# Optimization experiments

Hardware: AMD Instinct MI355X
Metric: run time of the kernel (lower is better)

The kernel has to match this reference:

```python
import jax, jax.numpy as jnp
import numpy as np

K, P, D = 9, 4, 1          # kernel_size, padding, dilation of each WeightedConv1D (stride=1)
SIGMA = 0.08               # WeightedConv1D default; the sigma arg of WeightedConv2D.forward is ignored
EPS = 1e-5                 # BatchNorm1d eps


def setup_inputs() -> dict:
    key = jax.random.key(0)
    ks = jax.random.split(key, 9)
    B, C, O, N = 4, 64, 64, 16384
    return {
        "input": jax.random.normal(ks[0], (B, C, N), jnp.float32),
        "multi_coords": jax.random.uniform(ks[1], (B, 3, N, 4), dtype=jnp.float32),
        "indices": jax.random.randint(ks[2], (B, N, 4), 0, N),
        "reindices": jax.random.randint(ks[3], (B, N, 4), 0, N),
        "conv_w": jax.random.normal(ks[4], (4, O, C, K), jnp.float32) * 0.05,   # 4 WeightedConv1D weights [O,C,K]
        "fusion_w": jax.random.normal(ks[5], (O, 4 * O), jnp.float32) * 0.05,   # Conv1d(4O -> O, kernel=1)
        "fusion_b": jax.random.normal(ks[6], (O,), jnp.float32) * 0.05,
        "bn_gamma": jnp.ones((O,), jnp.float32),
        "bn_beta": jnp.zeros((O,), jnp.float32),
    }


def _weighted_conv1d(x, coords, w):
    """x: [B,C,N], coords: [B,3,N], w: [O,C,K] -> [B,O,N] (L == N since P = D*(K-1)/2)."""
    N = x.shape[-1]
    win = jnp.arange(N)[None, :] + jnp.arange(K)[:, None] * D          # [K, N] window gather indices
    xw = jnp.pad(x, ((0, 0), (0, 0), (P, P)))[:, :, win]               # [B,C,K,N] == F.unfold layout
    cw = jnp.pad(coords, ((0, 0), (0, 0), (P, P)))[:, :, win]          # [B,3,K,N]
    diff = cw - cw[:, :, K // 2 : K // 2 + 1, :]                        # subtract window-center coord
    dw = jnp.maximum(1.0 - jnp.sqrt(jnp.sum(diff * diff, axis=1)) / SIGMA, 0.0)  # [B,K,N]
    return jnp.einsum('bckn,ock->bon', xw * dw[:, None], w)


def reference(input, multi_coords, indices, reindices, conv_w, fusion_w, fusion_b, bn_gamma, bn_beta):
    x = input
    outs = []
    for i in range(4):  # 4 space-filling-curve orderings; note x is reassigned (gathers compound)
        x = jnp.take_along_axis(x, indices[:, None, :, i], axis=2)      # [B,C,N]
        y = _weighted_conv1d(x, multi_coords[:, :, :, i], conv_w[i])    # [B,O,N]
        y = jnp.take_along_axis(y, reindices[:, None, :, i], axis=2)
        outs.append(y)
    cat = jnp.concatenate(outs, axis=1)                                 # [B,4O,N]
    # fusion: Conv1d(4O,O,kernel=1,padding=1,stride=1) -> padded positions see only bias
    z = jnp.einsum('bcn,oc->bon', cat, fusion_w)
    z = jnp.pad(z, ((0, 0), (0, 0), (1, 1))) + fusion_b[None, :, None]  # [B,O,N+2]
    # BatchNorm1d (training-mode batch statistics, biased variance)
    mean = jnp.mean(z, axis=(0, 2), keepdims=True)
    var = jnp.var(z, axis=(0, 2), keepdims=True)
    z = (z - mean) / jnp.sqrt(var + EPS) * bn_gamma[None, :, None] + bn_beta[None, :, None]
    return jax.nn.relu(z)
```

## Files before the change

kernel.cpp:

```cpp
#include <hip/hip_runtime.h>

#define K_ 9
#define SIGMA_INV 12.5f
#define EPS 1e-5f
#define B_ 4
#define C_ 64
#define O_ 64
#define N_ 16384
#define CAP 32768

typedef __attribute__((ext_vector_type(8))) short short8;
typedef __attribute__((ext_vector_type(4))) float f32x4;

__device__ __forceinline__ unsigned short f2bf(float f) {
    union { float f; unsigned u; } v; v.f = f;
    unsigned r = v.u + 0x7fffu + ((v.u >> 16) & 1u);
    return (unsigned short)(r >> 16);
}
__device__ __forceinline__ float bf2f(unsigned short h) {
    union { unsigned u; float f; } v; v.u = ((unsigned)h) << 16;
    return v.f;
}
__device__ __forceinline__ void gload16(const void* g, void* l) {
    __builtin_amdgcn_global_load_lds((const __attribute__((address_space(1))) unsigned int*)g,
                                     (__attribute__((address_space(3))) unsigned int*)l,
                                     16, 0, 0);
}

__global__ __launch_bounds__(256) void k_chain(const int* __restrict__ indices,
                                               const int* __restrict__ reidx,
                                               int* __restrict__ h,
                                               int* __restrict__ cnt) {
    int gid = blockIdx.x * 256 + threadIdx.x;
    if (gid == 0) *cnt = 0;
    int b = gid >> 14, n = gid & (N_ - 1);
    const int* ib = indices + (size_t)b * N_ * 4;
    const int4 r = *(const int4*)&reidx[((size_t)b * N_ + n) * 4];
    int t0 = ib[(size_t)r.x * 4 + 0];
    int t1 = ib[(size_t)r.y * 4 + 1];
    int t2 = ib[(size_t)r.z * 4 + 2];
    int t3 = ib[(size_t)r.w * 4 + 3];
    t1 = ib[(size_t)t1 * 4 + 0];
    t2 = ib[(size_t)t2 * 4 + 1];
    t3 = ib[(size_t)t3 * 4 + 2];
    t2 = ib[(size_t)t2 * 4 + 0];
    t3 = ib[(size_t)t3 * 4 + 1];
    t3 = ib[(size_t)t3 * 4 + 0];
    h[(size_t)(0 * 4 + b) * N_ + n] = t0;
    h[(size_t)(1 * 4 + b) * N_ + n] = t1;
    h[(size_t)(2 * 4 + b) * N_ + n] = t2;
    h[(size_t)(3 * 4 + b) * N_ + n] = t3;
}

__global__ __launch_bounds__(256) void k_setup(
    const float* __restrict__ in, const float* __restrict__ mc,
    const float* __restrict__ cw, const float* __restrict__ fw,
    unsigned short* __restrict__ xtb,
    unsigned short* __restrict__ Mfrag, float* __restrict__ Wt,
    float* __restrict__ FWt,
    int* __restrict__ flag, int* __restrict__ emeta,
    float* __restrict__ ed, int* __restrict__ cnt)
{
    int bid = blockIdx.x, t = threadIdx.x;
    if (bid < 1024) {
        __shared__ float tile[64][65];
        int b = bid & 3, n0 = (bid >> 2) * 64;
        for (int rep = 0; rep < 16; ++rep) {
            int idx = rep * 256 + t;
            int c = idx >> 6, j = idx & 63;
            tile[c][j] = in[((size_t)b * C_ + c) * N_ + n0 + j];
        }
        __syncthreads();
        for (int rep = 0; rep < 4; ++rep) {
            int idx = rep * 256 + t;
            int j = idx >> 4, c4 = (idx & 15) * 4;
            ushort4 o;
            o.x = f2bf(tile[c4 + 0][j]); o.y = f2bf(tile[c4 + 1][j]);
            o.z = f2bf(tile[c4 + 2][j]); o.w = f2bf(tile[c4 + 3][j]);
            *(ushort4*)&xtb[((size_t)b * N_ + n0 + j) * 64 + c4] = o;
        }
    } else if (bid < 1280) {
        __shared__ float cs[3][264][4];
        int sb = bid - 1024;
        int b = sb & 3, n0 = (sb >> 2) * 256;
        for (int idx = t; idx < 3 * 264; idx += 256) {
            int a = idx / 264, r = idx - a * 264;
            int m = n0 + r - 4;
            f32x4 v;
            if (m >= 0 && m < N_) v = *(const f32x4*)&mc[(((size_t)b * 3 + a) * N_ + m) * 4];
            else { v[0] = 1e9f; v[1] = 1e9f; v[2] = 1e9f; v[3] = 1e9f; }
            *(f32x4*)&cs[a][r][0] = v;
        }
        __syncthreads();
        int p = n0 + t;
        for (int i = 0; i < 4; ++i) {
            float c0 = cs[0][t + 4][i], c1 = cs[1][t + 4][i], c2 = cs[2][t + 4][i];
            float d[8]; bool any = false;
            #pragma unroll
            for (int kk = 0; kk < 8; ++kk) {
                int k = kk + (kk >= 4);
                float d0 = cs[0][t + k][i] - c0, d1 = cs[1][t + k][i] - c1,
                      d2 = cs[2][t + k][i] - c2;
                float dist = sqrtf(d0 * d0 + d1 * d1 + d2 * d2);
                float dd = 1.f - dist * SIGMA_INV;
                d[kk] = dd > 0.f ? dd : 0.f;
                any = any || (dd > 0.f);
            }
            int fv = 0;
            if (any) {
                int e = atomicAdd(cnt, 1);
                if (e < CAP) {
                    emeta[e] = ((i * 4 + b) << 14) | p;
                    #pragma unroll
                    for (int kk = 0; kk < 8; ++kk) ed[(size_t)e * 8 + kk] = d[kk];
                    fv = e + 1;
                }
            }
            flag[(size_t)(i * 4 + b) * N_ + p] = fv;
        }
    } else {
        int pb = bid - 1280;
        if (pb < 4) {
            __shared__ float w4[64][65];
            __shared__ float fws[64][65];
            int i = pb;
            for (int idx = t; idx < 4096; idx += 256) {
                int op = idx >> 6, c = idx & 63;
                w4[op][c]  = cw[(((size_t)(i * 64 + op)) * 64 + c) * 9 + 4];
                fws[op][c] = fw[(size_t)op * 256 + i * 64 + c];
            }
            __syncthreads();
            int o = t >> 2, cb = (t & 3) * 16;
            float acc[16];
            #pragma unroll
            for (int j = 0; j < 16; ++j) acc[j] = 0.f;
            for (int op = 0; op < 64; ++op) {
                float f = fws[o][op];
                #pragma unroll
                for (int j = 0; j < 16; ++j) acc[j] += f * w4[op][cb + j];
            }
            #pragma unroll
            for (int j = 0; j < 16; ++j) {
                int c = cb + j;
                int s = i * 2 + (c >> 5);
                int l = (((c >> 3) & 3) << 4) | (o & 15);
                int w_ = o >> 4;
                Mfrag[(((size_t)w_ * 8 + s) * 64 + l) * 8 + (c & 7)] = f2bf(acc[j]);
            }
        } else if (pb < 40) {
            int idx2 = pb - 4;
            int i = idx2 / 9, k = idx2 - i * 9;
            for (int idx = t; idx < 4096; idx += 256) {
                int c = idx >> 6, o = idx & 63;
                Wt[(size_t)(i * 9 + k) * 4096 + c * 64 + o] =
                    cw[(((size_t)(i * 64 + o)) * 64 + c) * 9 + k];
            }
        } else {
            int i = pb - 40;
            for (int idx = t; idx < 4096; idx += 256) {
                int c = idx >> 6, o = idx & 63;
                FWt[(size_t)(i * 64 + c) * 64 + o] = fw[(size_t)o * 256 + i * 64 + c];
            }
        }
    }
}

__global__ __launch_bounds__(64) void k_corr(
    const unsigned short* __restrict__ xtb, const int* __restrict__ indices,
    const float* __restrict__ Wt, const float* __restrict__ FWt,
    const int* __restrict__ emeta, const float* __restrict__ ed,
    const int* __restrict__ cnt, float* __restrict__ zcorr)
{
    __shared__ float xls[8][64];
    __shared__ float ycs[64];
    __shared__ int rows_s[8];
    int t = threadIdx.x;
    int n = *cnt; if (n > CAP) n = CAP;
    for (int e = blockIdx.x; e < n; e += gridDim.x) {
        int meta = emeta[e];
        int ibx = meta >> 14, p = meta & 16383;
        int i = ibx >> 2, b = ibx & 3;
        const int* idxb = indices + (size_t)b * N_ * 4;
        float dd[8];
        #pragma unroll
        for (int kk = 0; kk < 8; ++kk) dd[kk] = ed[(size_t)e * 8 + kk];
        if (t < 8) {
            int row = 0;
            if (dd[t] > 0.f) {
                int k = t + (t >= 4);
                int rr = p + k - 4;
                for (int s = i; s >= 0; --s) rr = idxb[(size_t)rr * 4 + s];
                row = rr;
            }
            rows_s[t] = row;
        }
        __syncthreads();
        #pragma unroll
        for (int kk = 0; kk < 8; ++kk) {
            if (dd[kk] > 0.f)
                xls[kk][t] = bf2f(xtb[((size_t)b * N_ + rows_s[kk]) * 64 + t]);
        }
        __syncthreads();
        float y = 0.f;
        #pragma unroll 1
        for (int kk = 0; kk < 8; ++kk) {
            if (dd[kk] > 0.f) {
                int k = kk + (kk >= 4);
                const float* w = Wt + (size_t)(i * 9 + k) * 4096;
                float s0 = 0.f, s1 = 0.f, s2 = 0.f, s3 = 0.f;
                #pragma unroll
                for (int c = 0; c < 64; c += 4) {
                    s0 += w[(c + 0) * 64 + t] * xls[kk][c + 0];
                    s1 += w[(c + 1) * 64 + t] * xls[kk][c + 1];
                    s2 += w[(c + 2) * 64 + t] * xls[kk][c + 2];
                    s3 += w[(c + 3) * 64 + t] * xls[kk][c + 3];
                }
                y += dd[kk] * (((s0 + s1) + (s2 + s3)));
            }
        }
        ycs[t] = y;
        __syncthreads();
        const float* fwt = FWt + (size_t)i * 4096;
        float v0 = 0.f, v1 = 0.f, v2 = 0.f, v3 = 0.f;
        #pragma unroll
        for (int c = 0; c < 64; c += 4) {
            v0 += fwt[(c + 0) * 64 + t] * ycs[c + 0];
            v1 += fwt[(c + 1) * 64 + t] * ycs[c + 1];
            v2 += fwt[(c + 2) * 64 + t] * ycs[c + 2];
            v3 += fwt[(c + 3) * 64 + t] * ycs[c + 3];
        }
        zcorr[(size_t)e * 64 + t] = (v0 + v1) + (v2 + v3);
        __syncthreads();
    }
}

__global__ __launch_bounds__(256) void k_fused(
    const unsigned short* __restrict__ xtb, const int* __restrict__ h,
    const int* __restrict__ flag, const int* __restrict__ reidx,
    const unsigned short* __restrict__ Mfrag, const float* __restrict__ zcorr,
    const float* __restrict__ fb, float* __restrict__ zbuf,
    float* __restrict__ pstats)
{
    __shared__ __align__(16) unsigned short xg[256 * 64];
    __shared__ int fs[256];
    int bid = blockIdx.x;
    int b = (bid & 7) >> 1;
    int nb = ((bid >> 3) << 1) | (bid & 1);
    int n0 = nb * 64;
    int t = threadIdx.x;
    int lane = t & 63, w = t >> 6;

    int hvv[8];
    #pragma unroll
    for (int it = 0; it < 8; ++it)
        hvv[it] = h[(size_t)(w * 4 + b) * N_ + n0 + it * 8 + (lane >> 3)];
    short8 af[8];
    #pragma unroll
    for (int s = 0; s < 8; ++s)
        af[s] = *(const short8*)&Mfrag[(((size_t)w * 8 + s) * 64 + lane) * 8];
    #pragma unroll
    for (int it = 0; it < 8; ++it) {
        int p = it * 8 + (lane >> 3);
        int cg = (lane & 7) ^ (p & 7);
        const unsigned short* gp = xtb + ((size_t)b * N_ + hvv[it]) * 64 + cg * 8;
        gload16(gp, &xg[(size_t)(w * 64 + it * 8) * 64]);
    }
    {
        int i = t >> 6, p = t & 63;
        int pr = reidx[((size_t)b * N_ + n0 + p) * 4 + i];
        fs[t] = flag[(size_t)(i * 4 + b) * N_ + pr];
    }
    asm volatile("s_waitcnt vmcnt(0)" ::: "memory");
    __syncthreads();

    f32x4 acc[4];
    #pragma unroll
    for (int ct = 0; ct < 4; ++ct) { acc[ct][0]=0.f; acc[ct][1]=0.f; acc[ct][2]=0.f; acc[ct][3]=0.f; }
    #pragma unroll
    for (int s = 0; s < 8; ++s) {
        int i2 = s >> 1;
        int cg = (s & 1) * 4 + (lane >> 4);
        #pragma unroll
        for (int ct = 0; ct < 4; ++ct) {
            int pos = ct * 16 + (lane & 15);
            const short8 bf = *(const short8*)((const char*)xg +
                ((size_t)(i2 * 64 + pos) * 128) + ((cg ^ (pos & 7)) * 16));
            acc[ct] = __builtin_amdgcn_mfma_f32_16x16x32_bf16(af[s], bf, acc[ct], 0, 0, 0);
        }
    }

    int og = w * 16 + (lane >> 4) * 4;
    const f32x4 bias4 = *(const f32x4*)&fb[og];
    float sums[4] = {0.f, 0.f, 0.f, 0.f}, sqs[4] = {0.f, 0.f, 0.f, 0.f};
    #pragma unroll
    for (int ct = 0; ct < 4; ++ct) {
        int p = ct * 16 + (lane & 15);
        #pragma unroll
        for (int i = 0; i < 4; ++i) {
            int f = fs[i * 64 + p];
            if (f > 0) {
                const f32x4 vc = *(const f32x4*)&zcorr[(size_t)(f - 1) * 64 + og];
                acc[ct] += vc;
            }
        }
        f32x4 z = acc[ct] + bias4;
        int n = n0 + p;
        #pragma unroll
        for (int r = 0; r < 4; ++r) {
            zbuf[((size_t)b * O_ + og + r) * N_ + n] = z[r];
            sums[r] += z[r]; sqs[r] += z[r] * z[r];
        }
    }
    #pragma unroll
    for (int r = 0; r < 4; ++r) {
        float s = sums[r], q = sqs[r];
        for (int m = 8; m >= 1; m >>= 1) {
            s += __shfl_xor(s, m);
            q += __shfl_xor(q, m);
        }
        if ((lane & 15) == 0) {
            pstats[(size_t)(og + r) * 1024 + bid] = s;
            pstats[(size_t)(64 + og + r) * 1024 + bid] = q;
        }
    }
}

__global__ __launch_bounds__(256) void k_bnstats(
    const float* __restrict__ pstats, const float* __restrict__ fb,
    const float* __restrict__ gamma, const float* __restrict__ beta,
    float* __restrict__ sc)
{
    __shared__ float ls[4], lq[4];
    int o = blockIdx.x, t = threadIdx.x;
    int lane = t & 63, w = t >> 6;
    float s = 0.f, q = 0.f;
    #pragma unroll
    for (int r = 0; r < 4; ++r) {
        s += pstats[(size_t)o * 1024 + r * 256 + t];
        q += pstats[(size_t)(64 + o) * 1024 + r * 256 + t];
    }
    #pragma unroll
    for (int m = 32; m >= 1; m >>= 1) {
        s += __shfl_xor(s, m);
        q += __shfl_xor(q, m);
    }
    if (lane == 0) { ls[w] = s; lq[w] = q; }
    __syncthreads();
    if (t == 0) {
        s = ls[0] + ls[1] + ls[2] + ls[3];
        q = lq[0] + lq[1] + lq[2] + lq[3];
        float cnt = (float)(B_ * (N_ + 2));
        float bias = fb[o];
        s += 2.f * B_ * bias;
        q += 2.f * B_ * bias * bias;
        float mean = s / cnt;
        float var = q / cnt - mean * mean;
        float scale = gamma[o] / sqrtf(var + EPS);
        sc[o] = scale;
        sc[O_ + o] = beta[o] - mean * scale;
    }
}

__global__ __launch_bounds__(256) void k_apply(const float* __restrict__ zbuf,
                                               const float* __restrict__ fb,
                                               const float* __restrict__ sc,
                                               float* __restrict__ out) {
    int bid = blockIdx.x, t = threadIdx.x;
    if (bid < 4096) {
        int gid = bid * 256 + t;
        int row = gid >> 12;
        int n = (gid & 4095) * 4;
        int o = row & 63;
        float scale = sc[o], shift = sc[O_ + o];
        f32x4 z = *(const f32x4*)&zbuf[(size_t)row * N_ + n];
        size_t ob = (size_t)row * (N_ + 2) + 1 + n;
        #pragma unroll
        for (int r = 0; r < 4; ++r)
            out[ob + r] = fmaxf(z[r] * scale + shift, 0.f);
    } else {
        int row = t;
        int o = row & 63;
        float v = fmaxf(fb[o] * sc[o] + sc[O_ + o], 0.f);
        out[(size_t)row * (N_ + 2)] = v;
        out[(size_t)row * (N_ + 2) + N_ + 1] = v;
    }
}

extern "C" void kernel_launch(void* const* d_in, const int* in_sizes, int n_in,
                              void* d_out, int out_size, void* d_ws, size_t ws_size,
                              hipStream_t stream) {
    const float* input   = (const float*)d_in[0];
    const float* mc      = (const float*)d_in[1];
    const int*   indices = (const int*)d_in[2];
    const int*   reidx   = (const int*)d_in[3];
    const float* cw      = (const float*)d_in[4];
    const float* fw      = (const float*)d_in[5];
    const float* fb      = (const float*)d_in[6];
    const float* gamma   = (const float*)d_in[7];
    const float* beta    = (const float*)d_in[8];
    float* out = (float*)d_out;

    char* ws = (char*)d_ws;
    size_t off = 0;
    auto alloc = [&](size_t bytes) { void* p = ws + off; off += (bytes + 255) & ~(size_t)255; return p; };
    unsigned short* xtb = (unsigned short*)alloc((size_t)B_ * N_ * C_ * 2);
    int*   h     = (int*)  alloc((size_t)4 * B_ * N_ * 4);
    unsigned short* Mfrag = (unsigned short*)alloc((size_t)4 * 8 * 64 * 8 * 2);
    float* Wt    = (float*)alloc((size_t)4 * 9 * 4096 * 4);
    float* FWt   = (float*)alloc((size_t)4 * 4096 * 4);
    int*   emeta = (int*)  alloc((size_t)CAP * 4);
    float* ed    = (float*)alloc((size_t)CAP * 8 * 4);
    float* zcorr = (float*)alloc((size_t)CAP * 64 * 4);
    float* zbuf  = (float*)alloc((size_t)B_ * O_ * N_ * 4);
    float* pstats= (float*)alloc((size_t)128 * 1024 * 4);
    float* sc    = (float*)alloc((size_t)128 * 4);
    int*   flag  = (int*)  alloc((size_t)4 * B_ * N_ * 4);
    int*   cnt   = (int*)  alloc(256);

    k_chain<<<256, 256, 0, stream>>>(indices, reidx, h, cnt);
    k_setup<<<1324, 256, 0, stream>>>(input, mc, cw, fw,
                                      xtb, Mfrag, Wt, FWt, flag, emeta, ed, cnt);
    k_corr<<<2048, 64, 0, stream>>>(xtb, indices, Wt, FWt, emeta, ed, cnt, zcorr);
    k_fused<<<1024, 256, 0, stream>>>(xtb, h, flag, reidx, Mfrag, zcorr, fb, zbuf, pstats);
    k_bnstats<<<64, 256, 0, stream>>>(pstats, fb, gamma, beta, sc);
    k_apply<<<4097, 256, 0, stream>>>(zbuf, fb, sc, out);
}
```

Measured before the change: 69.11 us.

## Fuse fusion GEMM, BN stats and apply into cooperative kernel with grid syncs

Merges the fused GEMM, batch-norm statistics and normalize/ReLU stages into one cooperative kernel that keeps accumulators in registers across two grid-wide syncs. This removes the full zbuf round trip through global memory and two kernel launches. It also folds the index-chain kernel into the setup kernel and swaps the single global atomic compaction counter for per-block local counters with fixed-capacity regions. The risks are that more than RCAP active points in one block are silently dropped, that grid-sync and occupancy requirements apply, and that a non-cooperative fallback path is kept.

```diff
diff --git a/kernel.cpp b/kernel.cpp
--- a/kernel.cpp
+++ b/kernel.cpp
@@ -1,4 +1,7 @@
 #include <hip/hip_runtime.h>
+#include <hip/hip_cooperative_groups.h>
+
+namespace cg = cooperative_groups;
 
 #define K_ 9
 #define SIGMA_INV 12.5f
@@ -7,7 +10,7 @@
 #define C_ 64
 #define O_ 64
 #define N_ 16384
-#define CAP 32768
+#define RCAP 128
 
 typedef __attribute__((ext_vector_type(8))) short short8;
 typedef __attribute__((ext_vector_type(4))) float f32x4;
@@ -27,39 +30,15 @@
                                      16, 0, 0);
 }
 
-__global__ __launch_bounds__(256) void k_chain(const int* __restrict__ indices,
-                                               const int* __restrict__ reidx,
-                                               int* __restrict__ h,
-                                               int* __restrict__ cnt) {
-    int gid = blockIdx.x * 256 + threadIdx.x;
-    if (gid == 0) *cnt = 0;
-    int b = gid >> 14, n = gid & (N_ - 1);
-    const int* ib = indices + (size_t)b * N_ * 4;
-    const int4 r = *(const int4*)&reidx[((size_t)b * N_ + n) * 4];
-    int t0 = ib[(size_t)r.x * 4 + 0];
-    int t1 = ib[(size_t)r.y * 4 + 1];
-    int t2 = ib[(size_t)r.z * 4 + 2];
-    int t3 = ib[(size_t)r.w * 4 + 3];
-    t1 = ib[(size_t)t1 * 4 + 0];
-    t2 = ib[(size_t)t2 * 4 + 1];
-    t3 = ib[(size_t)t3 * 4 + 2];
-    t2 = ib[(size_t)t2 * 4 + 0];
-    t3 = ib[(size_t)t3 * 4 + 1];
-    t3 = ib[(size_t)t3 * 4 + 0];
-    h[(size_t)(0 * 4 + b) * N_ + n] = t0;
-    h[(size_t)(1 * 4 + b) * N_ + n] = t1;
-    h[(size_t)(2 * 4 + b) * N_ + n] = t2;
-    h[(size_t)(3 * 4 + b) * N_ + n] = t3;
-}
-
 __global__ __launch_bounds__(256) void k_setup(
     const float* __restrict__ in, const float* __restrict__ mc,
+    const int* __restrict__ indices, const int* __restrict__ reidx,
     const float* __restrict__ cw, const float* __restrict__ fw,
-    unsigned short* __restrict__ xtb,
+    unsigned short* __restrict__ xtb, int* __restrict__ h,
     unsigned short* __restrict__ Mfrag, float* __restrict__ Wt,
     float* __restrict__ FWt,
     int* __restrict__ flag, int* __restrict__ emeta,
-    float* __restrict__ ed, int* __restrict__ cnt)
+    float* __restrict__ ed, int* __restrict__ bcnt)
 {
     int bid = blockIdx.x, t = threadIdx.x;
     if (bid < 1024) {
@@ -81,8 +60,10 @@
         }
     } else if (bid < 1280) {
         __shared__ float cs[3][264][4];
+        __shared__ int lcnt;
         int sb = bid - 1024;
         int b = sb & 3, n0 = (sb >> 2) * 256;
+        if (t == 0) lcnt = 0;
         for (int idx = t; idx < 3 * 264; idx += 256) {
             int a = idx / 264, r = idx - a * 264;
             int m = n0 + r - 4;
@@ -108,17 +89,20 @@
             }
             int fv = 0;
             if (any) {
-                int e = atomicAdd(cnt, 1);
-                if (e < CAP) {
-                    emeta[e] = ((i * 4 + b) << 14) | p;
+                int li = atomicAdd(&lcnt, 1);
+                if (li < RCAP) {
+                    int slot = sb * RCAP + li;
+                    emeta[slot] = (i << 14) | p;
                     #pragma unroll
-                    for (int kk = 0; kk < 8; ++kk) ed[(size_t)e * 8 + kk] = d[kk];
-                    fv = e + 1;
+                    for (int kk = 0; kk < 8; ++kk) ed[(size_t)slot * 8 + kk] = d[kk];
+                    fv = slot + 1;
                 }
             }
             flag[(size_t)(i * 4 + b) * N_ + p] = fv;
         }
-    } else {
+        __syncthreads();
+        if (t == 0) bcnt[sb] = lcnt < RCAP ? lcnt : RCAP;
+    } else if (bid < 1324) {
         int pb = bid - 1280;
         if (pb < 4) {
             __shared__ float w4[64][65];
@@ -162,6 +146,25 @@
                 FWt[(size_t)(i * 64 + c) * 64 + o] = fw[(size_t)o * 256 + i * 64 + c];
             }
         }
+    } else {
+        int gid = (bid - 1324) * 256 + t;
+        int b = gid >> 14, n = gid & (N_ - 1);
+        const int* ib = indices + (size_t)b * N_ * 4;
+        const int4 r = *(const int4*)&reidx[((size_t)b * N_ + n) * 4];
+        int t0 = ib[(size_t)r.x * 4 + 0];
+        int t1 = ib[(size_t)r.y * 4 + 1];
+        int t2 = ib[(size_t)r.z * 4 + 2];
+        int t3 = ib[(size_t)r.w * 4 + 3];
+        t1 = ib[(size_t)t1 * 4 + 0];
+        t2 = ib[(size_t)t2 * 4 + 1];
+        t3 = ib[(size_t)t3 * 4 + 2];
+        t2 = ib[(size_t)t2 * 4 + 0];
+        t3 = ib[(size_t)t3 * 4 + 1];
+        t3 = ib[(size_t)t3 * 4 + 0];
+        h[(size_t)(0 * 4 + b) * N_ + n] = t0;
+        h[(size_t)(1 * 4 + b) * N_ + n] = t1;
+        h[(size_t)(2 * 4 + b) * N_ + n] = t2;
+        h[(size_t)(3 * 4 + b) * N_ + n] = t3;
     }
 }
 
@@ -169,21 +172,23 @@
     const unsigned short* __restrict__ xtb, const int* __restrict__ indices,
     const float* __restrict__ Wt, const float* __restrict__ FWt,
     const int* __restrict__ emeta, const float* __restrict__ ed,
-    const int* __restrict__ cnt, float* __restrict__ zcorr)
+    const int* __restrict__ bcnt, float* __restrict__ zcorr)
 {
     __shared__ float xls[8][64];
     __shared__ float ycs[64];
     __shared__ int rows_s[8];
     int t = threadIdx.x;
-    int n = *cnt; if (n > CAP) n = CAP;
-    for (int e = blockIdx.x; e < n; e += gridDim.x) {
-        int meta = emeta[e];
-        int ibx = meta >> 14, p = meta & 16383;
-        int i = ibx >> 2, b = ibx & 3;
-        const int* idxb = indices + (size_t)b * N_ * 4;
+    int r = blockIdx.x >> 3, wir = blockIdx.x & 7;
+    int b = r & 3;
+    int cr = bcnt[r];
+    const int* idxb = indices + (size_t)b * N_ * 4;
+    for (int li = wir; li < cr; li += 8) {
+        int slot = r * RCAP + li;
+        int meta = emeta[slot];
+        int i = meta >> 14, p = meta & 16383;
         float dd[8];
         #pragma unroll
-        for (int kk = 0; kk < 8; ++kk) dd[kk] = ed[(size_t)e * 8 + kk];
+        for (int kk = 0; kk < 8; ++kk) dd[kk] = ed[(size_t)slot * 8 + kk];
         if (t < 8) {
             int row = 0;
             if (dd[t] > 0.f) {
@@ -229,12 +234,165 @@
             v2 += fwt[(c + 2) * 64 + t] * ycs[c + 2];
             v3 += fwt[(c + 3) * 64 + t] * ycs[c + 3];
         }
-        zcorr[(size_t)e * 64 + t] = (v0 + v1) + (v2 + v3);
-        __syncthreads();
-    }
-}
-
-__global__ __launch_bounds__(256) void k_fused(
+        zcorr[(size_t)slot * 64 + t] = (v0 + v1) + (v2 + v3);
+        __syncthreads();
+    }
+}
+
+__global__ __launch_bounds__(256, 2) void k_mega2(
+    const unsigned short* __restrict__ xtb, const int* __restrict__ h,
+    const int* __restrict__ flag, const int* __restrict__ reidx,
+    const unsigned short* __restrict__ Mfrag, const float* __restrict__ zcorr,
+    const float* __restrict__ fb, const float* __restrict__ gamma,
+    const float* __restrict__ beta, float* __restrict__ pstats,
+    float* __restrict__ sc, float* __restrict__ out)
+{
+    __shared__ __align__(16) unsigned short xg[2][256 * 64];
+    __shared__ int fs[2][256];
+    __shared__ float red_s[4], red_q[4];
+    int bid = blockIdx.x;
+    int b = bid & 3;
+    int base = (bid >> 2) * 128;
+    int t = threadIdx.x;
+    int lane = t & 63, w = t >> 6;
+
+    short8 af[8];
+    #pragma unroll
+    for (int s = 0; s < 8; ++s)
+        af[s] = *(const short8*)&Mfrag[(((size_t)w * 8 + s) * 64 + lane) * 8];
+    #pragma unroll
+    for (int j = 0; j < 2; ++j) {
+        int n0 = base + j * 64;
+        int hvv[8];
+        #pragma unroll
+        for (int it = 0; it < 8; ++it)
+            hvv[it] = h[(size_t)(w * 4 + b) * N_ + n0 + it * 8 + (lane >> 3)];
+        #pragma unroll
+        for (int it = 0; it < 8; ++it) {
+            int p = it * 8 + (lane >> 3);
+            int cg = (lane & 7) ^ (p & 7);
+            const unsigned short* gp = xtb + ((size_t)b * N_ + hvv[it]) * 64 + cg * 8;
+            gload16(gp, &xg[j][(size_t)(w * 64 + it * 8) * 64]);
+        }
+        {
+            int i = t >> 6, p = t & 63;
+            int pr = reidx[((size_t)b * N_ + n0 + p) * 4 + i];
+            fs[j][t] = flag[(size_t)(i * 4 + b) * N_ + pr];
+        }
+    }
+    asm volatile("s_waitcnt vmcnt(0)" ::: "memory");
+    __syncthreads();
+
+    f32x4 acc[2][4];
+    #pragma unroll
+    for (int j = 0; j < 2; ++j)
+        #pragma unroll
+        for (int ct = 0; ct < 4; ++ct) { acc[j][ct][0]=0.f; acc[j][ct][1]=0.f; acc[j][ct][2]=0.f; acc[j][ct][3]=0.f; }
+    #pragma unroll
+    for (int j = 0; j < 2; ++j)
+        #pragma unroll
+        for (int s = 0; s < 8; ++s) {
+            int i2 = s >> 1;
+            int cg = (s & 1) * 4 + (lane >> 4);
+            #pragma unroll
+            for (int ct = 0; ct < 4; ++ct) {
+                int pos = ct * 16 + (lane & 15);
+                const short8 bf = *(const short8*)((const char*)&xg[j][0] +
+                    ((size_t)(i2 * 64 + pos) * 128) + ((cg ^ (pos & 7)) * 16));
+                acc[j][ct] = __builtin_amdgcn_mfma_f32_16x16x32_bf16(af[s], bf, acc[j][ct], 0, 0, 0);
+            }
+        }
+
+    int og = w * 16 + (lane >> 4) * 4;
+    const f32x4 bias4 = *(const f32x4*)&fb[og];
+    float sums[4] = {0.f, 0.f, 0.f, 0.f}, sqs[4] = {0.f, 0.f, 0.f, 0.f};
+    #pragma unroll
+    for (int j = 0; j < 2; ++j)
+        #pragma unroll
+        for (int ct = 0; ct < 4; ++ct) {
+            int p = ct * 16 + (lane & 15);
+            #pragma unroll
+            for (int i = 0; i < 4; ++i) {
+                int f = fs[j][i * 64 + p];
+                if (f > 0) {
+                    const f32x4 vc = *(const f32x4*)&zcorr[(size_t)(f - 1) * 64 + og];
+                    acc[j][ct] += vc;
+                }
+            }
+            acc[j][ct] += bias4;
+            #pragma unroll
+            for (int r = 0; r < 4; ++r) { sums[r] += acc[j][ct][r]; sqs[r] += acc[j][ct][r] * acc[j][ct][r]; }
+        }
+    #pragma unroll
+    for (int r = 0; r < 4; ++r) {
+        float s = sums[r], q = sqs[r];
+        for (int m = 8; m >= 1; m >>= 1) {
+            s += __shfl_xor(s, m);
+            q += __shfl_xor(q, m);
+        }
+        if ((lane & 15) == 0) {
+            pstats[(size_t)(og + r) * 512 + bid] = s;
+            pstats[(size_t)(64 + og + r) * 512 + bid] = q;
+        }
+    }
+
+    __threadfence();
+    cg::this_grid().sync();
+
+    if (bid < 64) {
+        float s = 0.f, q = 0.f;
+        #pragma unroll
+        for (int rp = 0; rp < 2; ++rp) {
+            s += pstats[(size_t)bid * 512 + rp * 256 + t];
+            q += pstats[(size_t)(64 + bid) * 512 + rp * 256 + t];
+        }
+        #pragma unroll
+        for (int m = 32; m >= 1; m >>= 1) {
+            s += __shfl_xor(s, m);
+            q += __shfl_xor(q, m);
+        }
+        if (lane == 0) { red_s[w] = s; red_q[w] = q; }
+        __syncthreads();
+        if (t == 0) {
+            s = red_s[0] + red_s[1] + red_s[2] + red_s[3];
+            q = red_q[0] + red_q[1] + red_q[2] + red_q[3];
+            float cntf = (float)(B_ * (N_ + 2));
+            float bias = fb[bid];
+            s += 2.f * B_ * bias;
+            q += 2.f * B_ * bias * bias;
+            float mean = s / cntf;
+            float var = q / cntf - mean * mean;
+            float scale = gamma[bid] / sqrtf(var + EPS);
+            sc[bid] = scale;
+            sc[64 + bid] = beta[bid] - mean * scale;
+        }
+    }
+
+    __threadfence();
+    cg::this_grid().sync();
+
+    const f32x4 scl4 = *(const f32x4*)&sc[og];
+    const f32x4 sft4 = *(const f32x4*)&sc[64 + og];
+    #pragma unroll
+    for (int j = 0; j < 2; ++j)
+        #pragma unroll
+        for (int ct = 0; ct < 4; ++ct) {
+            int n = base + j * 64 + ct * 16 + (lane & 15);
+            #pragma unroll
+            for (int r = 0; r < 4; ++r) {
+                float v = fmaxf(acc[j][ct][r] * scl4[r] + sft4[r], 0.f);
+                out[(size_t)(b * 64 + og + r) * (N_ + 2) + 1 + n] = v;
+            }
+        }
+    if (bid == 64) {
+        int o = t & 63;
+        float v = fmaxf(fb[o] * sc[o] + sc[64 + o], 0.f);
+        out[(size_t)t * (N_ + 2)] = v;
+        out[(size_t)t * (N_ + 2) + N_ + 1] = v;
+    }
+}
+
+__global__ __launch_bounds__(256) void k_fused_fb(
     const unsigned short* __restrict__ xtb, const int* __restrict__ h,
     const int* __restrict__ flag, const int* __restrict__ reidx,
     const unsigned short* __restrict__ Mfrag, const float* __restrict__ zcorr,
@@ -325,7 +483,7 @@
     }
 }
 
-__global__ __launch_bounds__(256) void k_bnstats(
+__global__ __launch_bounds__(256) void k_bnstats_fb(
     const float* __restrict__ pstats, const float* __restrict__ fb,
     const float* __restrict__ gamma, const float* __restrict__ beta,
     float* __restrict__ sc)
@@ -361,10 +519,10 @@
     }
 }
 
-__global__ __launch_bounds__(256) void k_apply(const float* __restrict__ zbuf,
-                                               const float* __restrict__ fb,
-                                               const float* __restrict__ sc,
-                                               float* __restrict__ out) {
+__global__ __launch_bounds__(256) void k_apply_fb(const float* __restrict__ zbuf,
+                                                  const float* __restrict__ fb,
+                                                  const float* __restrict__ sc,
+                                                  float* __restrict__ out) {
     int bid = blockIdx.x, t = threadIdx.x;
     if (bid < 4096) {
         int gid = bid * 256 + t;
@@ -408,20 +566,40 @@
     unsigned short* Mfrag = (unsigned short*)alloc((size_t)4 * 8 * 64 * 8 * 2);
     float* Wt    = (float*)alloc((size_t)4 * 9 * 4096 * 4);
     float* FWt   = (float*)alloc((size_t)4 * 4096 * 4);
-    int*   emeta = (int*)  alloc((size_t)CAP * 4);
-    float* ed    = (float*)alloc((size_t)CAP * 8 * 4);
-    float* zcorr = (float*)alloc((size_t)CAP * 64 * 4);
-    float* zbuf  = (float*)alloc((size_t)B_ * O_ * N_ * 4);
+    int*   emeta = (int*)  alloc((size_t)256 * RCAP * 4);
+    float* ed    = (float*)alloc((size_t)256 * RCAP * 8 * 4);
+    float* zcorr = (float*)alloc((size_t)256 * RCAP * 64 * 4);
     float* pstats= (float*)alloc((size_t)128 * 1024 * 4);
     float* sc    = (float*)alloc((size_t)128 * 4);
     int*   flag  = (int*)  alloc((size_t)4 * B_ * N_ * 4);
-    int*   cnt   = (int*)  alloc(256);
-
-    k_chain<<<256, 256, 0, stream>>>(indices, reidx, h, cnt);
-    k_setup<<<1324, 256, 0, stream>>>(input, mc, cw, fw,
-                                      xtb, Mfrag, Wt, FWt, flag, emeta, ed, cnt);
-    k_corr<<<2048, 64, 0, stream>>>(xtb, indices, Wt, FWt, emeta, ed, cnt, zcorr);
-    k_fused<<<1024, 256, 0, stream>>>(xtb, h, flag, reidx, Mfrag, zcorr, fb, zbuf, pstats);
-    k_bnstats<<<64, 256, 0, stream>>>(pstats, fb, gamma, beta, sc);
-    k_apply<<<4097, 256, 0, stream>>>(zbuf, fb, sc, out);
-}
+    int*   bcnt  = (int*)  alloc((size_t)256 * 4);
+    float* zbuf  = (float*)alloc((size_t)B_ * O_ * N_ * 4);
+
+    k_setup<<<1580, 256, 0, stream>>>(input, mc, indices, reidx, cw, fw,
+                                      xtb, h, Mfrag, Wt, FWt, flag, emeta, ed, bcnt);
+    k_corr<<<2048, 64, 0, stream>>>(xtb, indices, Wt, FWt, emeta, ed, bcnt, zcorr);
+
+    bool coop = false;
+    int maxb = 0;
+    if (hipOccupancyMaxActiveBlocksPerMultiprocessor(
+            &maxb, (const void*)k_mega2, 256, 0) == hipSuccess) {
+        int dev = 0, cus = 0;
+        hipGetDevice(&dev);
+        hipDeviceGetAttribute(&cus, hipDeviceAttributeMultiprocessorCount, dev);
+        if ((long)maxb * (long)cus >= 512) coop = true;
+    }
+    if (coop) {
+        void* params[] = {(void*)&xtb, (void*)&h, (void*)&flag, (void*)&reidx,
+                          (void*)&Mfrag, (void*)&zcorr, (void*)&fb, (void*)&gamma,
+                          (void*)&beta, (void*)&pstats, (void*)&sc, (void*)&out};
+        if (hipLaunchCooperativeKernel((const void*)k_mega2, dim3(512), dim3(256),
+                                       params, 0, stream) != hipSuccess)
+            coop = false;
+    }
+    if (!coop) {
+        k_fused_fb<<<1024, 256, 0, stream>>>(xtb, h, flag, reidx, Mfrag, zcorr,
+                                             fb, zbuf, pstats);
+        k_bnstats_fb<<<64, 256, 0, stream>>>(pstats, fb, gamma, beta, sc);
+        k_apply_fb<<<4097, 256, 0, stream>>>(zbuf, fb, sc, out);
+    }
+}
```

Result: slower. 262.9 us (+280.3%).

## Merge chain into setup, per-block correction slots, bf16 intermediate z buffer

Applied to the files above, without the earlier changes.

Folds the index-chain kernel into the setup kernel as extra blocks, which removes one launch. The global atomic counter for correction entries becomes a per-block shared counter with fixed 128-slot regions, and k_corr is remapped to read those regions, so there is no global atomic contention. The intermediate z buffer is stored as bf16 to halve its write and read traffic, and the padded boundary outputs move into k_bnstats. The risks are bf16 rounding of pre-normalization values and silently dropped corrections if any block overflows 128 entries.

```diff
diff --git a/kernel.cpp b/kernel.cpp
--- a/kernel.cpp
+++ b/kernel.cpp
@@ -7,9 +7,10 @@
 #define C_ 64
 #define O_ 64
 #define N_ 16384
-#define CAP 32768
+#define RCAP 128
 
 typedef __attribute__((ext_vector_type(8))) short short8;
+typedef __attribute__((ext_vector_type(8))) unsigned short ushort8;
 typedef __attribute__((ext_vector_type(4))) float f32x4;
 
 __device__ __forceinline__ unsigned short f2bf(float f) {
@@ -27,39 +28,15 @@
                                      16, 0, 0);
 }
 
-__global__ __launch_bounds__(256) void k_chain(const int* __restrict__ indices,
-                                               const int* __restrict__ reidx,
-                                               int* __restrict__ h,
-                                               int* __restrict__ cnt) {
-    int gid = blockIdx.x * 256 + threadIdx.x;
-    if (gid == 0) *cnt = 0;
-    int b = gid >> 14, n = gid & (N_ - 1);
-    const int* ib = indices + (size_t)b * N_ * 4;
-    const int4 r = *(const int4*)&reidx[((size_t)b * N_ + n) * 4];
-    int t0 = ib[(size_t)r.x * 4 + 0];
-    int t1 = ib[(size_t)r.y * 4 + 1];
-    int t2 = ib[(size_t)r.z * 4 + 2];
-    int t3 = ib[(size_t)r.w * 4 + 3];
-    t1 = ib[(size_t)t1 * 4 + 0];
-    t2 = ib[(size_t)t2 * 4 + 1];
-    t3 = ib[(size_t)t3 * 4 + 2];
-    t2 = ib[(size_t)t2 * 4 + 0];
-    t3 = ib[(size_t)t3 * 4 + 1];
-    t3 = ib[(size_t)t3 * 4 + 0];
-    h[(size_t)(0 * 4 + b) * N_ + n] = t0;
-    h[(size_t)(1 * 4 + b) * N_ + n] = t1;
-    h[(size_t)(2 * 4 + b) * N_ + n] = t2;
-    h[(size_t)(3 * 4 + b) * N_ + n] = t3;
-}
-
 __global__ __launch_bounds__(256) void k_setup(
     const float* __restrict__ in, const float* __restrict__ mc,
+    const int* __restrict__ indices, const int* __restrict__ reidx,
     const float* __restrict__ cw, const float* __restrict__ fw,
-    unsigned short* __restrict__ xtb,
+    unsigned short* __restrict__ xtb, int* __restrict__ h,
     unsigned short* __restrict__ Mfrag, float* __restrict__ Wt,
     float* __restrict__ FWt,
     int* __restrict__ flag, int* __restrict__ emeta,
-    float* __restrict__ ed, int* __restrict__ cnt)
+    float* __restrict__ ed, int* __restrict__ bcnt)
 {
     int bid = blockIdx.x, t = threadIdx.x;
     if (bid < 1024) {
@@ -81,8 +58,10 @@
         }
     } else if (bid < 1280) {
         __shared__ float cs[3][264][4];
+        __shared__ int lcnt;
         int sb = bid - 1024;
         int b = sb & 3, n0 = (sb >> 2) * 256;
+        if (t == 0) lcnt = 0;
         for (int idx = t; idx < 3 * 264; idx += 256) {
             int a = idx / 264, r = idx - a * 264;
             int m = n0 + r - 4;
@@ -108,17 +87,20 @@
             }
             int fv = 0;
             if (any) {
-                int e = atomicAdd(cnt, 1);
-                if (e < CAP) {
-                    emeta[e] = ((i * 4 + b) << 14) | p;
+                int li = atomicAdd(&lcnt, 1);
+                if (li < RCAP) {
+                    int slot = sb * RCAP + li;
+                    emeta[slot] = (i << 14) | p;
                     #pragma unroll
-                    for (int kk = 0; kk < 8; ++kk) ed[(size_t)e * 8 + kk] = d[kk];
-                    fv = e + 1;
+                    for (int kk = 0; kk < 8; ++kk) ed[(size_t)slot * 8 + kk] = d[kk];
+                    fv = slot + 1;
                 }
             }
             flag[(size_t)(i * 4 + b) * N_ + p] = fv;
         }
-    } else {
+        __syncthreads();
+        if (t == 0) bcnt[sb] = lcnt < RCAP ? lcnt : RCAP;
+    } else if (bid < 1324) {
         int pb = bid - 1280;
         if (pb < 4) {
             __shared__ float w4[64][65];
@@ -162,6 +144,25 @@
                 FWt[(size_t)(i * 64 + c) * 64 + o] = fw[(size_t)o * 256 + i * 64 + c];
             }
         }
+    } else {
+        int gid = (bid - 1324) * 256 + t;
+        int b = gid >> 14, n = gid & (N_ - 1);
+        const int* ib = indices + (size_t)b * N_ * 4;
+        const int4 r = *(const int4*)&reidx[((size_t)b * N_ + n) * 4];
+        int t0 = ib[(size_t)r.x * 4 + 0];
+        int t1 = ib[(size_t)r.y * 4 + 1];
+        int t2 = ib[(size_t)r.z * 4 + 2];
+        int t3 = ib[(size_t)r.w * 4 + 3];
+        t1 = ib[(size_t)t1 * 4 + 0];
+        t2 = ib[(size_t)t2 * 4 + 1];
+        t3 = ib[(size_t)t3 * 4 + 2];
+        t2 = ib[(size_t)t2 * 4 + 0];
+        t3 = ib[(size_t)t3 * 4 + 1];
+        t3 = ib[(size_t)t3 * 4 + 0];
+        h[(size_t)(0 * 4 + b) * N_ + n] = t0;
+        h[(size_t)(1 * 4 + b) * N_ + n] = t1;
+        h[(size_t)(2 * 4 + b) * N_ + n] = t2;
+        h[(size_t)(3 * 4 + b) * N_ + n] = t3;
     }
 }
 
@@ -169,21 +170,23 @@
     const unsigned short* __restrict__ xtb, const int* __restrict__ indices,
     const float* __restrict__ Wt, const float* __restrict__ FWt,
     const int* __restrict__ emeta, const float* __restrict__ ed,
-    const int* __restrict__ cnt, float* __restrict__ zcorr)
+    const int* __restrict__ bcnt, float* __restrict__ zcorr)
 {
     __shared__ float xls[8][64];
     __shared__ float ycs[64];
     __shared__ int rows_s[8];
     int t = threadIdx.x;
-    int n = *cnt; if (n > CAP) n = CAP;
-    for (int e = blockIdx.x; e < n; e += gridDim.x) {
-        int meta = emeta[e];
-        int ibx = meta >> 14, p = meta & 16383;
-        int i = ibx >> 2, b = ibx & 3;
-        const int* idxb = indices + (size_t)b * N_ * 4;
+    int r = blockIdx.x >> 3, wir = blockIdx.x & 7;
+    int b = r & 3;
+    int cr = bcnt[r];
+    const int* idxb = indices + (size_t)b * N_ * 4;
+    for (int li = wir; li < cr; li += 8) {
+        int slot = r * RCAP + li;
+        int meta = emeta[slot];
+        int i = meta >> 14, p = meta & 16383;
         float dd[8];
         #pragma unroll
-        for (int kk = 0; kk < 8; ++kk) dd[kk] = ed[(size_t)e * 8 + kk];
+        for (int kk = 0; kk < 8; ++kk) dd[kk] = ed[(size_t)slot * 8 + kk];
         if (t < 8) {
             int row = 0;
             if (dd[t] > 0.f) {
@@ -229,7 +232,7 @@
             v2 += fwt[(c + 2) * 64 + t] * ycs[c + 2];
             v3 += fwt[(c + 3) * 64 + t] * ycs[c + 3];
         }
-        zcorr[(size_t)e * 64 + t] = (v0 + v1) + (v2 + v3);
+        zcorr[(size_t)slot * 64 + t] = (v0 + v1) + (v2 + v3);
         __syncthreads();
     }
 }
@@ -238,7 +241,7 @@
     const unsigned short* __restrict__ xtb, const int* __restrict__ h,
     const int* __restrict__ flag, const int* __restrict__ reidx,
     const unsigned short* __restrict__ Mfrag, const float* __restrict__ zcorr,
-    const float* __restrict__ fb, float* __restrict__ zbuf,
+    const float* __restrict__ fb, unsigned short* __restrict__ zbuf,
     float* __restrict__ pstats)
 {
     __shared__ __align__(16) unsigned short xg[256 * 64];
@@ -307,7 +310,7 @@
         int n = n0 + p;
         #pragma unroll
         for (int r = 0; r < 4; ++r) {
-            zbuf[((size_t)b * O_ + og + r) * N_ + n] = z[r];
+            zbuf[((size_t)b * O_ + og + r) * N_ + n] = f2bf(z[r]);
             sums[r] += z[r]; sqs[r] += z[r] * z[r];
         }
     }
@@ -328,7 +331,7 @@
 __global__ __launch_bounds__(256) void k_bnstats(
     const float* __restrict__ pstats, const float* __restrict__ fb,
     const float* __restrict__ gamma, const float* __restrict__ beta,
-    float* __restrict__ sc)
+    float* __restrict__ sc, float* __restrict__ out)
 {
     __shared__ float ls[4], lq[4];
     int o = blockIdx.x, t = threadIdx.x;
@@ -358,32 +361,28 @@
         float scale = gamma[o] / sqrtf(var + EPS);
         sc[o] = scale;
         sc[O_ + o] = beta[o] - mean * scale;
-    }
-}
-
-__global__ __launch_bounds__(256) void k_apply(const float* __restrict__ zbuf,
-                                               const float* __restrict__ fb,
+        float pv = fmaxf(bias * scale + (beta[o] - mean * scale), 0.f);
+        #pragma unroll
+        for (int b = 0; b < B_; ++b) {
+            out[(size_t)(b * O_ + o) * (N_ + 2)] = pv;
+            out[(size_t)(b * O_ + o) * (N_ + 2) + N_ + 1] = pv;
+        }
+    }
+}
+
+__global__ __launch_bounds__(256) void k_apply(const unsigned short* __restrict__ zbuf,
                                                const float* __restrict__ sc,
                                                float* __restrict__ out) {
-    int bid = blockIdx.x, t = threadIdx.x;
-    if (bid < 4096) {
-        int gid = bid * 256 + t;
-        int row = gid >> 12;
-        int n = (gid & 4095) * 4;
-        int o = row & 63;
-        float scale = sc[o], shift = sc[O_ + o];
-        f32x4 z = *(const f32x4*)&zbuf[(size_t)row * N_ + n];
-        size_t ob = (size_t)row * (N_ + 2) + 1 + n;
-        #pragma unroll
-        for (int r = 0; r < 4; ++r)
-            out[ob + r] = fmaxf(z[r] * scale + shift, 0.f);
-    } else {
-        int row = t;
-        int o = row & 63;
-        float v = fmaxf(fb[o] * sc[o] + sc[O_ + o], 0.f);
-        out[(size_t)row * (N_ + 2)] = v;
-        out[(size_t)row * (N_ + 2) + N_ + 1] = v;
-    }
+    int gid = blockIdx.x * 256 + threadIdx.x;
+    int row = gid >> 11;
+    int n = (gid & 2047) * 8;
+    int o = row & 63;
+    float scale = sc[o], shift = sc[O_ + o];
+    ushort8 z = *(const ushort8*)&zbuf[(size_t)row * N_ + n];
+    size_t ob = (size_t)row * (N_ + 2) + 1 + n;
+    #pragma unroll
+    for (int r = 0; r < 8; ++r)
+        out[ob + r] = fmaxf(bf2f(z[r]) * scale + shift, 0.f);
 }
 
 extern "C" void kernel_launch(void* const* d_in, const int* in_sizes, int n_in,
@@ -408,20 +407,20 @@
     unsigned short* Mfrag = (unsigned short*)alloc((size_t)4 * 8 * 64 * 8 * 2);
     float* Wt    = (float*)alloc((size_t)4 * 9 * 4096 * 4);
     float* FWt   = (float*)alloc((size_t)4 * 4096 * 4);
-    int*   emeta = (int*)  alloc((size_t)CAP * 4);
-    float* ed    = (float*)alloc((size_t)CAP * 8 * 4);
-    float* zcorr = (float*)alloc((size_t)CAP * 64 * 4);
-    float* zbuf  = (float*)alloc((size_t)B_ * O_ * N_ * 4);
+    int*   emeta = (int*)  alloc((size_t)256 * RCAP * 4);
+    float* ed    = (float*)alloc((size_t)256 * RCAP * 8 * 4);
+    float* zcorr = (float*)alloc((size_t)256 * RCAP * 64 * 4);
     float* pstats= (float*)alloc((size_t)128 * 1024 * 4);
     float* sc    = (float*)alloc((size_t)128 * 4);
     int*   flag  = (int*)  alloc((size_t)4 * B_ * N_ * 4);
-    int*   cnt   = (int*)  alloc(256);
-
-    k_chain<<<256, 256, 0, stream>>>(indices, reidx, h, cnt);
-    k_setup<<<1324, 256, 0, stream>>>(input, mc, cw, fw,
-                                      xtb, Mfrag, Wt, FWt, flag, emeta, ed, cnt);
-    k_corr<<<2048, 64, 0, stream>>>(xtb, indices, Wt, FWt, emeta, ed, cnt, zcorr);
-    k_fused<<<1024, 256, 0, stream>>>(xtb, h, flag, reidx, Mfrag, zcorr, fb, zbuf, pstats);
-    k_bnstats<<<64, 256, 0, stream>>>(pstats, fb, gamma, beta, sc);
-    k_apply<<<4097, 256, 0, stream>>>(zbuf, fb, sc, out);
-}
+    int*   bcnt  = (int*)  alloc((size_t)256 * 4);
+    unsigned short* zbuf = (unsigned short*)alloc((size_t)B_ * O_ * N_ * 2);
+
+    k_setup<<<1580, 256, 0, stream>>>(input, mc, indices, reidx, cw, fw,
+                                      xtb, h, Mfrag, Wt, FWt, flag, emeta, ed, bcnt);
+    k_corr<<<2048, 64, 0, stream>>>(xtb, indices, Wt, FWt, emeta, ed, bcnt, zcorr);
+    k_fused<<<1024, 256, 0, stream>>>(xtb, h, flag, reidx, Mfrag, zcorr,
+                                      fb, zbuf, pstats);
+    k_bnstats<<<64, 256, 0, stream>>>(pstats, fb, gamma, beta, sc, out);
+    k_apply<<<2048, 256, 0, stream>>>(zbuf, sc, out);
+}
```

Result: faster. 57.45 us (-16.9%).
